# Performance work log

Hardware: AMD Instinct MI355X
Metric: run time of the kernel (lower is better)

The kernel has to match this reference:

```python
import jax, jax.numpy as jnp
import numpy as np

B, G, D, H, L, MLP = 64, 512, 384, 6, 12, 4
DH = D // H
MASK_RATIO = 0.6
KEEP_RATIO = 0.1
PAD_VAL = -1.0
START_VAL = 1.0
POS_HID = 128
NEG = -1e9


def setup_inputs() -> dict:
    key = jax.random.key(0)
    ks = jax.random.split(key, 24)
    s = 0.02
    inp = {
        "x": jax.random.normal(ks[0], (B, G, D), jnp.float32),
        "center_points": jax.random.normal(ks[1], (B, G, 3), jnp.float32),
        "mask_noise": jax.random.uniform(ks[2], (B, G), jnp.float32),
        # pos embedder MLP: 3 -> 128 -> D
        "pos_w1": jax.random.normal(ks[3], (3, POS_HID), jnp.float32) * s,
        "pos_b1": jnp.zeros((POS_HID,), jnp.float32),
        "pos_w2": jax.random.normal(ks[4], (POS_HID, D), jnp.float32) * s,
        "pos_b2": jnp.zeros((D,), jnp.float32),
        # stacked per-layer transformer params
        "ln1_w": jnp.ones((L, D), jnp.float32),
        "ln1_b": jnp.zeros((L, D), jnp.float32),
        "qkv_w": jax.random.normal(ks[5], (L, D, 3 * D), jnp.float32) * s,
        "qkv_b": jnp.zeros((L, 3 * D), jnp.float32),
        "proj_w": jax.random.normal(ks[6], (L, D, D), jnp.float32) * s,
        "proj_b": jnp.zeros((L, D), jnp.float32),
        "ln2_w": jnp.ones((L, D), jnp.float32),
        "ln2_b": jnp.zeros((L, D), jnp.float32),
        "fc1_w": jax.random.normal(ks[7], (L, D, MLP * D), jnp.float32) * s,
        "fc1_b": jnp.zeros((L, MLP * D), jnp.float32),
        "fc2_w": jax.random.normal(ks[8], (L, MLP * D, D), jnp.float32) * s,
        "fc2_b": jnp.zeros((L, D), jnp.float32),
        # final LayerNorm
        "norm_w": jnp.ones((D,), jnp.float32),
        "norm_b": jnp.zeros((D,), jnp.float32),
    }
    return inp


def _layer_norm(h, w, b, eps=1e-5):
    mu = jnp.mean(h, axis=-1, keepdims=True)
    var = jnp.mean(jnp.square(h - mu), axis=-1, keepdims=True)
    return (h - mu) * jax.lax.rsqrt(var + eps) * w + b


def _random_mask(center, noise):
    # padding tokens: all coords equal PAD_VAL
    pad = jnp.all(center == PAD_VAL, axis=-1)                      # [B, G] bool
    if MASK_RATIO == 0:
        return jnp.zeros(pad.shape, bool), pad
    n = (G - jnp.sum(pad.astype(jnp.int32), axis=-1))              # non-padding count
    k = (n.astype(jnp.float32) * KEEP_RATIO).astype(jnp.int32)     # kept-first tokens
    m = ((n - k).astype(jnp.float32) * MASK_RATIO).astype(jnp.int32)
    M = jnp.max(m)
    j = jnp.arange(G)[None, :]
    # shuffle region [k, n): pick m random slots (uniform subset via rank of noise)
    region = (j >= k[:, None]) & (j < n[:, None])
    u = jnp.where(region, noise, jnp.inf)
    rank = jnp.argsort(jnp.argsort(u, axis=-1), axis=-1)
    shuf = (rank < m[:, None]) & region
    # tail of ones: positions [n, n + M - m)
    tail = (j >= n[:, None]) & (j < (n + M - m)[:, None])
    return shuf | tail, pad


def _attention(h, qw, qb, pw, pb, bias):
    qkv = (h @ qw + qb).reshape(B, G, 3, H, DH).transpose(2, 0, 3, 1, 4)
    q, k, v = qkv[0], qkv[1], qkv[2]                               # [B, H, G, DH]
    s = jnp.einsum('bhqd,bhkd->bhqk', q, k) * (DH ** -0.5) + bias
    a = jax.nn.softmax(s, axis=-1)
    o = jnp.einsum('bhqk,bhkd->bhqd', a, v).transpose(0, 2, 1, 3).reshape(B, G, D)
    return o @ pw + pb


def _forward(x, center_points, mask_noise,
             pos_w1, pos_b1, pos_w2, pos_b2,
             ln1_w, ln1_b, qkv_w, qkv_b, proj_w, proj_b,
             ln2_w, ln2_b, fc1_w, fc1_b, fc2_w, fc2_b,
             norm_w, norm_b):
    # shift right + start token
    start = jnp.full((B, 1, D), START_VAL, x.dtype)
    x = jnp.concatenate([start, x[:, :-1, :]], axis=1)
    # positional embedding of shifted centers + start-token pos
    pos = jax.nn.gelu(center_points[:, :-1, :] @ pos_w1 + pos_b1, approximate=False) @ pos_w2 + pos_b2
    pos = jnp.concatenate([jnp.full((B, 1, D), START_VAL, x.dtype), pos], axis=1)
    # causal | (random column mask & ~eye) attention mask
    triu = jnp.triu(jnp.ones((G, G), bool), 1)
    rand_mask, pad = _random_mask(center_points, mask_noise)
    eye = jnp.eye(G, dtype=bool)
    attn_mask = triu[None, :, :] | (rand_mask[:, None, :] & ~eye[None, :, :])   # [B, G, G]
    bias = jnp.where(attn_mask | pad[:, None, :], NEG, 0.0)[:, None, :, :]      # [B,1,G,G]

    def block(h, p):
        l1w, l1b, qw, qb, pw, pb, l2w, l2b, f1w, f1b, f2w, f2b = p
        h = h + pos
        h = h + _attention(_layer_norm(h, l1w, l1b), qw, qb, pw, pb, bias)
        h = h + (jax.nn.gelu(_layer_norm(h, l2w, l2b) @ f1w + f1b, approximate=False) @ f2w + f2b)
        return h, None

    x, _ = jax.lax.scan(block, x, (ln1_w, ln1_b, qkv_w, qkv_b, proj_w, proj_b,
                                   ln2_w, ln2_b, fc1_w, fc1_b, fc2_w, fc2_b))
    x = _layer_norm(x, norm_w, norm_b)
    return x, pad, attn_mask


def reference(x, center_points, mask_noise,
              pos_w1, pos_b1, pos_w2, pos_b2,
              ln1_w, ln1_b, qkv_w, qkv_b, proj_w, proj_b,
              ln2_w, ln2_b, fc1_w, fc1_b, fc2_w, fc2_b,
              norm_w, norm_b):
    out, pad, attn_mask = _forward(x, center_points, mask_noise,
                                   pos_w1, pos_b1, pos_w2, pos_b2,
                                   ln1_w, ln1_b, qkv_w, qkv_b, proj_w, proj_b,
                                   ln2_w, ln2_b, fc1_w, fc1_b, fc2_w, fc2_b,
                                   norm_w, norm_b)
    # torch repeat_interleave over heads -> [B*H, G, G]
    return out, pad, jnp.repeat(attn_mask, H, axis=0)
```

## Files before the change

### kernel.cpp

```cpp
#include <hip/hip_runtime.h>
#include <math.h>

typedef _Float16 f16;
typedef f16 f16x8 __attribute__((ext_vector_type(8)));
typedef f16 f16v2 __attribute__((ext_vector_type(2)));
typedef float f32x4 __attribute__((ext_vector_type(4)));

#define NB 64
#define NG 512
#define ND 384
#define NH 6
#define NL 12
#define NDH 64
#define BG (NB * NG)
#define BGD (BG * ND)

#define OFF_WQKV   0
#define OFF_WPROJ  2654208
#define OFF_WFC1   3538944
#define OFF_WFC2   7077888
#define OFF_FLAGS  10616832
#define OFF_NKM    10625024
#define OFF_MMAX   10625216
#define OFF_POS    10625280
#define OFF_HID    23208192
#define OFF_Y      25305344
#define OFF_YBIG   31596800
#define OFF_QB     56762624
#define OFF_KB     63054080
#define OFF_VT     69345536
#define OFF_OB     75636992
#define OFF_W2T    81928448
#define OFF_HB     81953024

typedef __attribute__((address_space(3))) void lds_t;
typedef const __attribute__((address_space(1))) void gmem_t;
__device__ __forceinline__ void gload16(const void* g, void* l)
{
    __builtin_amdgcn_global_load_lds((gmem_t*)g, (lds_t*)l, 16, 0, 0);
}

__global__ __launch_bounds__(256)
void transpose_kernel(const float* __restrict__ src, f16* __restrict__ dst,
                      int K, int N)
{
    __shared__ float tile[32][33];
    const int l = blockIdx.z;
    const float* S = src + (size_t)l * K * N;
    f16* D = dst + (size_t)l * K * N;
    const int n0 = blockIdx.x * 32, k0 = blockIdx.y * 32;
    const int tx = threadIdx.x, ty = threadIdx.y;
#pragma unroll
    for (int i = 0; i < 32; i += 8)
        tile[ty + i][tx] = S[(size_t)(k0 + ty + i) * N + n0 + tx];
    __syncthreads();
#pragma unroll
    for (int i = 0; i < 32; i += 8)
        D[(size_t)(n0 + ty + i) * K + k0 + tx] = (f16)tile[tx][ty + i];
}

__global__ __launch_bounds__(256)
void dpos_a(const float* cen, const float* w1, const float* b1, f16* hid)
{
    const int idx = blockIdx.x * 256 + threadIdx.x;
    if (idx >= BG * 128) return;
    const int t = idx >> 7, k = idx & 127;
    const int g = t & (NG - 1);
    if (g == 0) { hid[idx] = (f16)0.f; return; }
    const float* c = cen + (size_t)(t - 1) * 3;
    const float hv = c[0] * w1[k] + c[1] * w1[128 + k] + c[2] * w1[256 + k] + b1[k];
    hid[idx] = (f16)(0.5f * hv * (1.0f + erff(hv * 0.70710678118654752f)));
}

__global__ __launch_bounds__(384)
void pos_fix(f16* pos)
{
    const int b = blockIdx.x;
    pos[((size_t)b * NG) * ND + threadIdx.x] = (f16)1.0f;
}

__global__ __launch_bounds__(512)
void dmask_a(const float* cen, float* pad_out, int* nkm)
{
    const int b = blockIdx.x, j = threadIdx.x;
    const float* c = cen + ((size_t)b * NG + j) * 3;
    const bool pad = (c[0] == -1.f) && (c[1] == -1.f) && (c[2] == -1.f);
    pad_out[b * NG + j] = pad ? 1.f : 0.f;
    if (j == 0) {
        int cnt = 0;
        for (int i = 0; i < NG; i++) {
            const float* ci = cen + ((size_t)b * NG + i) * 3;
            cnt += (ci[0] == -1.f && ci[1] == -1.f && ci[2] == -1.f) ? 1 : 0;
        }
        const int n = NG - cnt;
        const int k = (int)((float)n * 0.1f);
        const int m = (int)((float)(n - k) * 0.6f);
        nkm[b * 3] = n; nkm[b * 3 + 1] = k; nkm[b * 3 + 2] = m;
    }
}

__global__ void dmask_m(const int* nkm, int* Mmax)
{
    if (threadIdx.x == 0 && blockIdx.x == 0) {
        int M = 0;
        for (int b = 0; b < NB; b++) M = max(M, nkm[b * 3 + 2]);
        *Mmax = M;
    }
}

__global__ __launch_bounds__(512)
void dmask_b(const float* cen, const float* noi, const int* nkm,
             const int* Mmax, unsigned char* flags)
{
    const int b = blockIdx.x, j = threadIdx.x;
    const int n = nkm[b * 3], k = nkm[b * 3 + 1], m = nkm[b * 3 + 2];
    const int M = *Mmax;
    const float nz = noi[b * NG + j];
    const bool inreg = (j >= k) && (j < n);
    bool shuf = false;
    if (inreg) {
        int cnt = 0;
        for (int i = 0; i < NG; i++) {
            if (i < k || i >= n) continue;
            const float ui = noi[b * NG + i];
            cnt += (ui < nz) || (ui == nz && i < j);
        }
        shuf = cnt < m;
    }
    const float* c = cen + ((size_t)b * NG + j) * 3;
    const bool pad = (c[0] == -1.f) && (c[1] == -1.f) && (c[2] == -1.f);
    const bool tail = (j >= n) && (j < n + M - m);
    flags[b * NG + j] = (unsigned char)(((shuf | tail) ? 1 : 0) | (pad ? 2 : 0));
}

__global__ __launch_bounds__(512)
void flags_rep_kernel(const unsigned char* flags, float* mo)
{
    const int bq = blockIdx.x;
    const int b = bq >> 9, q = bq & (NG - 1);
    const int j = threadIdx.x;
    mo[(((size_t)(b * NH) * NG + q) * NG) + j] = (float)flags[b * NG + j];
}

__global__ __launch_bounds__(512)
void mask_out_kernel(float* mo)
{
    const int bq = blockIdx.x;
    const int b = bq >> 9, q = bq & (NG - 1);
    const int j = threadIdx.x;
    const unsigned char f =
        (unsigned char)mo[(((size_t)(b * NH) * NG + q) * NG) + j];
    const float val = ((q < j) || ((f & 1) && (q != j))) ? 1.0f : 0.0f;
#pragma unroll
    for (int h = 0; h < NH; h++)
        mo[(((size_t)(b * NH + h) * NG + q) * NG) + j] = val;
}

__global__ __launch_bounds__(256)
void h0_kernel(const float* x, const f16* pos, f16* h)
{
    const size_t i = (size_t)blockIdx.x * 256 + threadIdx.x;
    const int g = (int)((i / ND) & (NG - 1));
    const float xv = x[(g == 0) ? i : (i - ND)];
    const float base = (g == 0) ? 1.0f : xv;
    h[i] = (f16)(base + (float)pos[i]);
}

template<int MODE>
__global__ __launch_bounds__(256)
void lnb_kernel(const f16* __restrict__ h,
                const float* __restrict__ w, const float* __restrict__ bb,
                f16* __restrict__ y16, float* __restrict__ y32)
{
    __shared__ float red[4][64];
    const int wid = threadIdx.x >> 6;
    const int lane = threadIdx.x & 63;
    const int t = blockIdx.x * 4 + wid;
    const size_t base = (size_t)t * ND + lane;
    float v[6];
    float s = 0.f;
#pragma unroll
    for (int i = 0; i < 6; i++) {
        const float xv = (float)h[base + i * 64];
        v[i] = xv; s += xv;
    }
    red[wid][lane] = s;
    __syncthreads();
    for (int st = 32; st > 0; st >>= 1) {
        if (lane < st) red[wid][lane] += red[wid][lane + st];
        __syncthreads();
    }
    const float mu = red[wid][0] * (1.f / ND);
    float vs = 0.f;
#pragma unroll
    for (int i = 0; i < 6; i++) { const float d = v[i] - mu; vs += d * d; }
    __syncthreads();
    red[wid][lane] = vs;
    __syncthreads();
    for (int st = 32; st > 0; st >>= 1) {
        if (lane < st) red[wid][lane] += red[wid][lane + st];
        __syncthreads();
    }
    const float rstd = rsqrtf(red[wid][0] * (1.f / ND) + 1e-5f);
#pragma unroll
    for (int i = 0; i < 6; i++) {
        const float o = (v[i] - mu) * rstd * w[lane + i * 64] + bb[lane + i * 64];
        if constexpr (MODE == 2) y32[base + i * 64] = o;
        else                     y16[base + i * 64] = (f16)o;
    }
}

template<int MODE>
__global__ __launch_bounds__(256)
void gemm_kernel(const f16* __restrict__ A, const f16* __restrict__ Bt,
                 const float* __restrict__ bias, int K, int NT,
                 f16* __restrict__ hres, f16* __restrict__ out16,
                 f16* __restrict__ Qo, f16* __restrict__ Ko, f16* __restrict__ Vo)
{
    __shared__ f16 sA[128 * 64];
    __shared__ f16 sB[128 * 64];
    const int tid = threadIdx.x;
    const int w = tid >> 6, lane = tid & 63;
    const int lr = lane & 15, lg = lane >> 4;
    const int wm = w >> 1, wn = w & 1;
    const int N = NT * 128;

    const int nwg = gridDim.x;
    const int chunk = nwg >> 3;
    const int flat = (blockIdx.x & 7) * chunk + (blockIdx.x >> 3);
    const int m0 = (flat / NT) * 128;
    const int n0 = (flat % NT) * 128;

    f32x4 acc[4][4];
#pragma unroll
    for (int mf = 0; mf < 4; mf++)
#pragma unroll
        for (int nf = 0; nf < 4; nf++)
            acc[mf][nf] = (f32x4){0.f, 0.f, 0.f, 0.f};

    const int srow0 = w * 8 + (lane >> 3);
    const int scolB = (lane & 7) * 16;

    for (int k0 = 0; k0 < K; k0 += 64) {
        __syncthreads();
#pragma unroll
        for (int i = 0; i < 4; i++) {
            const int row = i * 32 + srow0;
            const int colB = scolB ^ ((row & 7) << 4);
            const char* ga = (const char*)(A + (size_t)(m0 + row) * K + k0) + colB;
            const char* gb = (const char*)(Bt + (size_t)(n0 + row) * K + k0) + colB;
            gload16(ga, (char*)sA + row * 128 + scolB);
            gload16(gb, (char*)sB + row * 128 + scolB);
        }
        __syncthreads();
#pragma unroll
        for (int kk = 0; kk < 64; kk += 32) {
            f16x8 af[4], bf[4];
#pragma unroll
            for (int mf = 0; mf < 4; mf++) {
                const int r = wm * 64 + mf * 16 + lr;
                const int cb = ((kk + lg * 8) * 2) ^ ((r & 7) << 4);
                af[mf] = *(const f16x8*)((const char*)sA + r * 128 + cb);
            }
#pragma unroll
            for (int nf = 0; nf < 4; nf++) {
                const int r = wn * 64 + nf * 16 + lr;
                const int cb = ((kk + lg * 8) * 2) ^ ((r & 7) << 4);
                bf[nf] = *(const f16x8*)((const char*)sB + r * 128 + cb);
            }
#pragma unroll
            for (int mf = 0; mf < 4; mf++)
#pragma unroll
                for (int nf = 0; nf < 4; nf++)
                    acc[mf][nf] = __builtin_amdgcn_mfma_f32_16x16x32_f16(
                        af[mf], bf[nf], acc[mf][nf], 0, 0, 0);
        }
    }

#pragma unroll
    for (int mf = 0; mf < 4; mf++) {
#pragma unroll
        for (int nf = 0; nf < 4; nf++) {
            const int n_g = n0 + wn * 64 + nf * 16 + lr;
            const float bv = bias[n_g];
#pragma unroll
            for (int r = 0; r < 4; r++) {
                const int m_g = m0 + wm * 64 + mf * 16 + lg * 4 + r;
                const float v = acc[mf][nf][r] + bv;
                const size_t oidx = (size_t)m_g * N + n_g;
                if constexpr (MODE == 1) {
                    hres[oidx] = (f16)((float)hres[oidx] + v);
                } else if constexpr (MODE == 2) {
                    const float ge = 0.5f * v * (1.0f + erff(v * 0.70710678118654752f));
                    out16[oidx] = (f16)ge;
                } else if constexpr (MODE == 3) {
                    out16[oidx] = (f16)v;
                } else {
                    const int which = n_g / ND;
                    const int rem = n_g - which * ND;
                    const int hh = rem >> 6, dh = rem & 63;
                    const int bb2 = m_g >> 9, gg = m_g & (NG - 1);
                    if (which == 0)
                        Qo[((size_t)(bb2 * NH + hh) * NG + gg) * NDH + dh] = (f16)v;
                    else if (which == 1)
                        Ko[((size_t)(bb2 * NH + hh) * NG + gg) * NDH + dh] = (f16)v;
                    else
                        Vo[((size_t)(bb2 * NH + hh) * NDH + dh) * NG + gg] = (f16)v;
                }
            }
        }
    }
}

template<int ADDPOS>
__global__ __launch_bounds__(512)
void gemmln_kernel(const f16* __restrict__ A, const f16* __restrict__ Bt,
                   const float* __restrict__ bias, int K,
                   f16* __restrict__ hres, const f16* __restrict__ posadd,
                   const float* __restrict__ lw, const float* __restrict__ lb,
                   f16* __restrict__ Y)
{
    __shared__ f16 sA[128 * 64];
    __shared__ f16 sB[384 * 64];
    __shared__ float part[2][128][2];
    const int tid = threadIdx.x;
    const int w = tid >> 6, lane = tid & 63;
    const int lr = lane & 15, lg = lane >> 4;
    const int vm = w >> 1, vn = w & 1;

    const int nwg = gridDim.x;
    const int chunk = nwg >> 3;
    const int m0 = ((blockIdx.x & 7) * chunk + (blockIdx.x >> 3)) * 128;

    f32x4 acc[2][12];
#pragma unroll
    for (int mf = 0; mf < 2; mf++)
#pragma unroll
        for (int nf = 0; nf < 12; nf++)
            acc[mf][nf] = (f32x4){0.f, 0.f, 0.f, 0.f};

    const int srowA = tid >> 3;
    const int scolB = (tid & 7) * 16;

    for (int k0 = 0; k0 < K; k0 += 64) {
        __syncthreads();
#pragma unroll
        for (int i = 0; i < 2; i++) {
            const int row = i * 64 + srowA;
            const int colB = scolB ^ ((row & 7) << 4);
            gload16((const char*)(A + (size_t)(m0 + row) * K + k0) + colB,
                    (char*)sA + row * 128 + scolB);
        }
#pragma unroll
        for (int i = 0; i < 6; i++) {
            const int row = i * 64 + srowA;
            const int colB = scolB ^ ((row & 7) << 4);
            gload16((const char*)(Bt + (size_t)row * K + k0) + colB,
                    (char*)sB + row * 128 + scolB);
        }
        __syncthreads();
#pragma unroll
        for (int kk = 0; kk < 64; kk += 32) {
            f16x8 af[2];
#pragma unroll
            for (int mf = 0; mf < 2; mf++) {
                const int r = vm * 32 + mf * 16 + lr;
                const int cb = ((kk + lg * 8) * 2) ^ ((r & 7) << 4);
                af[mf] = *(const f16x8*)((const char*)sA + r * 128 + cb);
            }
#pragma unroll
            for (int half = 0; half < 2; half++) {
                f16x8 bf[6];
#pragma unroll
                for (int j = 0; j < 6; j++) {
                    const int nf = half * 6 + j;
                    const int r = vn * 192 + nf * 16 + lr;
                    const int cb = ((kk + lg * 8) * 2) ^ ((r & 7) << 4);
                    bf[j] = *(const f16x8*)((const char*)sB + r * 128 + cb);
                }
#pragma unroll
                for (int mf = 0; mf < 2; mf++)
#pragma unroll
                    for (int j = 0; j < 6; j++)
                        acc[mf][half * 6 + j] = __builtin_amdgcn_mfma_f32_16x16x32_f16(
                            af[mf], bf[j], acc[mf][half * 6 + j], 0, 0, 0);
            }
        }
    }

    f16v2 hn[2][12][2];
    float rs[2][4], rq[2][4];
#pragma unroll
    for (int mf = 0; mf < 2; mf++)
#pragma unroll
        for (int r = 0; r < 4; r++) { rs[mf][r] = 0.f; rq[mf][r] = 0.f; }

#pragma unroll
    for (int mf = 0; mf < 2; mf++) {
#pragma unroll
        for (int nf = 0; nf < 12; nf++) {
            const int col = vn * 192 + nf * 16 + lr;
            const float bv = bias[col];
#pragma unroll
            for (int r = 0; r < 4; r++) {
                const int row_g = m0 + vm * 32 + mf * 16 + lg * 4 + r;
                const size_t oidx = (size_t)row_g * ND + col;
                float hv = (float)hres[oidx] + acc[mf][nf][r] + bv;
                if constexpr (ADDPOS) hv += (float)posadd[oidx];
                const f16 hf = (f16)hv;
                hn[mf][nf][r >> 1][r & 1] = hf;
                const float hff = (float)hf;
                rs[mf][r] += hff;
                rq[mf][r] += hff * hff;
            }
        }
    }
#pragma unroll
    for (int mf = 0; mf < 2; mf++)
#pragma unroll
        for (int r = 0; r < 4; r++) {
#pragma unroll
            for (int off = 1; off < 16; off <<= 1) {
                rs[mf][r] += __shfl_xor(rs[mf][r], off);
                rq[mf][r] += __shfl_xor(rq[mf][r], off);
            }
        }
    if (lr == 0) {
#pragma unroll
        for (int mf = 0; mf < 2; mf++)
#pragma unroll
            for (int r = 0; r < 4; r++) {
                const int rl = vm * 32 + mf * 16 + lg * 4 + r;
                part[vn][rl][0] = rs[mf][r];
                part[vn][rl][1] = rq[mf][r];
            }
    }
    __syncthreads();

    float mus[2][4], rstds[2][4];
#pragma unroll
    for (int mf = 0; mf < 2; mf++)
#pragma unroll
        for (int r = 0; r < 4; r++) {
            const int rl = vm * 32 + mf * 16 + lg * 4 + r;
            const float s = part[0][rl][0] + part[1][rl][0];
            const float q = part[0][rl][1] + part[1][rl][1];
            const float mu = s * (1.f / ND);
            const float var = q * (1.f / ND) - mu * mu;
            mus[mf][r] = mu;
            rstds[mf][r] = rsqrtf(var + 1e-5f);
        }

#pragma unroll
    for (int mf = 0; mf < 2; mf++) {
#pragma unroll
        for (int nf = 0; nf < 12; nf++) {
            const int col = vn * 192 + nf * 16 + lr;
            const float wl = lw[col];
            const float bl = lb[col];
#pragma unroll
            for (int r = 0; r < 4; r++) {
                const int row_g = m0 + vm * 32 + mf * 16 + lg * 4 + r;
                const size_t oidx = (size_t)row_g * ND + col;
                const f16 hf = hn[mf][nf][r >> 1][r & 1];
                hres[oidx] = hf;
                const float o = ((float)hf - mus[mf][r]) * rstds[mf][r] * wl + bl;
                Y[oidx] = (f16)o;
            }
        }
    }
}

__global__ __launch_bounds__(256)
void attn_kernel(const f16* __restrict__ Q, const f16* __restrict__ Kt,
                 const f16* __restrict__ V, const unsigned char* __restrict__ flags,
                 f16* __restrict__ O)
{
    __shared__ f16 sQ[128][72];
    __shared__ f16 sK[64][72];
    __shared__ f16 sV[64][72];
    __shared__ f16 sP[4][16][72];
    const int tid = threadIdx.x;
    const int w = tid >> 6, lane = tid & 63;
    const int lr = lane & 15, lg = lane >> 4;
    const int q0 = blockIdx.x * 128;
    const int bh = blockIdx.y;
    const int b = bh / NH, hh = bh - b * NH;
    const f16* Qg = Q + ((size_t)bh * NG + q0) * NDH;
    const f16* Kg = Kt + (size_t)bh * NG * NDH;
    const f16* Vg = V + (size_t)bh * NDH * NG;
    const unsigned char* fl = flags + b * NG;

#pragma unroll
    for (int i = 0; i < 4; i++) {
        const int c = tid + i * 256;
        const int r = c >> 3, cc = (c & 7) * 8;
        *(f16x8*)&sQ[r][cc] = *(const f16x8*)(Qg + r * NDH + cc);
    }
    __syncthreads();
    f16x8 aq[2][2];
#pragma unroll
    for (int hf = 0; hf < 2; hf++) {
        aq[hf][0] = *(const f16x8*)&sQ[hf * 64 + w * 16 + lr][lg * 8];
        aq[hf][1] = *(const f16x8*)&sQ[hf * 64 + w * 16 + lr][32 + lg * 8];
    }

    float m_run[2][4], l_run[2][4];
    f32x4 o[2][4];
#pragma unroll
    for (int hf = 0; hf < 2; hf++)
#pragma unroll
        for (int r = 0; r < 4; r++) {
            m_run[hf][r] = -INFINITY; l_run[hf][r] = 0.f;
            o[hf][r] = (f32x4){0.f, 0.f, 0.f, 0.f};
        }

    const int ntile = 2 * blockIdx.x + 2;
    for (int jt = 0; jt < ntile; jt++) {
        const int j0 = jt * 64;
        __syncthreads();
#pragma unroll
        for (int i = 0; i < 2; i++) {
            const int c = tid + i * 256;
            const int r = c >> 3, cc = (c & 7) * 8;
            *(f16x8*)&sK[r][cc] = *(const f16x8*)(Kg + (size_t)(j0 + r) * NDH + cc);
            *(f16x8*)&sV[r][cc] = *(const f16x8*)(Vg + (size_t)r * NG + j0 + cc);
        }
        __syncthreads();

#pragma unroll
        for (int hf = 0; hf < 2; hf++) {
            if (jt >= ntile - 1 + hf) continue;
            f32x4 s[4];
#pragma unroll
            for (int nf = 0; nf < 4; nf++) s[nf] = (f32x4){0.f, 0.f, 0.f, 0.f};
#pragma unroll
            for (int kf = 0; kf < 2; kf++) {
#pragma unroll
                for (int nf = 0; nf < 4; nf++) {
                    f16x8 bk = *(const f16x8*)&sK[nf * 16 + lr][kf * 32 + lg * 8];
                    s[nf] = __builtin_amdgcn_mfma_f32_16x16x32_f16(aq[hf][kf], bk, s[nf], 0, 0, 0);
                }
            }
#pragma unroll
            for (int nf = 0; nf < 4; nf++) {
                const int j_g = j0 + nf * 16 + lr;
                const unsigned char f = fl[j_g];
#pragma unroll
                for (int r = 0; r < 4; r++) {
                    const int q_g = q0 + hf * 64 + w * 16 + lg * 4 + r;
                    const bool masked = (q_g < j_g) || (f & 2) || ((f & 1) && (j_g != q_g));
                    s[nf][r] = s[nf][r] * 0.125f + (masked ? -1e9f : 0.f);
                }
            }
#pragma unroll
            for (int r = 0; r < 4; r++) {
                float mx = fmaxf(fmaxf(s[0][r], s[1][r]), fmaxf(s[2][r], s[3][r]));
#pragma unroll
                for (int off = 1; off < 16; off <<= 1) mx = fmaxf(mx, __shfl_xor(mx, off));
                const float nm = fmaxf(m_run[hf][r], mx);
                const float sc = __expf(m_run[hf][r] - nm);
                m_run[hf][r] = nm;
                l_run[hf][r] *= sc;
#pragma unroll
                for (int nf = 0; nf < 4; nf++) o[hf][nf][r] *= sc;
                float ls = 0.f;
#pragma unroll
                for (int nf = 0; nf < 4; nf++) {
                    const float p = __expf(s[nf][r] - nm);
                    ls += p;
                    sP[w][lg * 4 + r][nf * 16 + lr] = (f16)p;
                }
                l_run[hf][r] += ls;
            }
#pragma unroll
            for (int kf = 0; kf < 2; kf++) {
                f16x8 ap = *(const f16x8*)&sP[w][lr][kf * 32 + lg * 8];
#pragma unroll
                for (int nf = 0; nf < 4; nf++) {
                    f16x8 bv = *(const f16x8*)&sV[nf * 16 + lr][kf * 32 + lg * 8];
                    o[hf][nf] = __builtin_amdgcn_mfma_f32_16x16x32_f16(ap, bv, o[hf][nf], 0, 0, 0);
                }
            }
        }
    }

#pragma unroll
    for (int hf = 0; hf < 2; hf++) {
        float inv[4];
#pragma unroll
        for (int r = 0; r < 4; r++) {
            float l = l_run[hf][r];
#pragma unroll
            for (int off = 1; off < 16; off <<= 1) l += __shfl_xor(l, off);
            inv[r] = 1.f / l;
        }
#pragma unroll
        for (int nf = 0; nf < 4; nf++) {
#pragma unroll
            for (int r = 0; r < 4; r++) {
                const int q_g = q0 + hf * 64 + w * 16 + lg * 4 + r;
                const int dh = nf * 16 + lr;
                O[((size_t)(b * NG + q_g)) * ND + hh * NDH + dh] = (f16)(o[hf][nf][r] * inv[r]);
            }
        }
    }
}

extern "C" void kernel_launch(void* const* d_in, const int* in_sizes, int n_in,
                              void* d_out, int out_size, void* d_ws, size_t ws_size,
                              hipStream_t stream)
{
    (void)d_ws; (void)ws_size;

    static const int exp_sizes[21] = {
        12582912, 98304, 32768,
        384, 128, 49152, 384,
        4608, 4608,
        5308416, 13824,
        1769472, 4608,
        4608, 4608,
        7077888, 18432,
        7077888, 4608,
        384, 384
    };
    if (n_in != 21 || out_size != 113278976) return;
    for (int i = 0; i < 21; i++) if (in_sizes[i] != exp_sizes[i]) return;

    const float* x    = (const float*)d_in[0];
    const float* cen  = (const float*)d_in[1];
    const float* noi  = (const float*)d_in[2];
    const float* pw1  = (const float*)d_in[3];
    const float* pb1  = (const float*)d_in[4];
    const float* pw2  = (const float*)d_in[5];
    const float* pb2  = (const float*)d_in[6];
    const float* ln1w = (const float*)d_in[7];
    const float* ln1b = (const float*)d_in[8];
    const float* qkvw = (const float*)d_in[9];
    const float* qkvb = (const float*)d_in[10];
    const float* projw= (const float*)d_in[11];
    const float* projb= (const float*)d_in[12];
    const float* ln2w = (const float*)d_in[13];
    const float* ln2b = (const float*)d_in[14];
    const float* fc1w = (const float*)d_in[15];
    const float* fc1b = (const float*)d_in[16];
    const float* fc2w = (const float*)d_in[17];
    const float* fc2b = (const float*)d_in[18];
    const float* nw   = (const float*)d_in[19];
    const float* nb   = (const float*)d_in[20];

    float* out0    = (float*)d_out;
    float* pad_out = out0 + BGD;
    float* R       = pad_out + BG;

    f16* WqkvT  = (f16*)(R + OFF_WQKV);
    f16* WprojT = (f16*)(R + OFF_WPROJ);
    f16* Wfc1T  = (f16*)(R + OFF_WFC1);
    f16* Wfc2T  = (f16*)(R + OFF_WFC2);
    unsigned char* flags = (unsigned char*)(R + OFF_FLAGS);
    int* nkm  = (int*)(R + OFF_NKM);
    int* Mmax = (int*)(R + OFF_MMAX);
    f16* POS   = (f16*)(R + OFF_POS);
    f16* HID   = (f16*)(R + OFF_HID);
    f16* Y     = (f16*)(R + OFF_Y);
    f16* Ybig  = (f16*)(R + OFF_YBIG);
    f16* Qb    = (f16*)(R + OFF_QB);
    f16* Kb    = (f16*)(R + OFF_KB);
    f16* Vt    = (f16*)(R + OFF_VT);
    f16* Ob    = (f16*)(R + OFF_OB);
    f16* W2T   = (f16*)(R + OFF_W2T);
    f16* Hb    = (f16*)(R + OFF_HB);

    dim3 tb(32, 8);
    transpose_kernel<<<dim3(36, 12, NL), tb, 0, stream>>>(qkvw, WqkvT, 384, 1152);
    transpose_kernel<<<dim3(12, 12, NL), tb, 0, stream>>>(projw, WprojT, 384, 384);
    transpose_kernel<<<dim3(48, 12, NL), tb, 0, stream>>>(fc1w, Wfc1T, 384, 1536);
    transpose_kernel<<<dim3(12, 48, NL), tb, 0, stream>>>(fc2w, Wfc2T, 1536, 384);
    transpose_kernel<<<dim3(12, 4, 1),  tb, 0, stream>>>(pw2, W2T, 128, 384);

    dmask_a<<<NB, 512, 0, stream>>>(cen, pad_out, nkm);
    dmask_m<<<1, 64, 0, stream>>>(nkm, Mmax);
    dmask_b<<<NB, 512, 0, stream>>>(cen, noi, nkm, Mmax, flags);
    dpos_a<<<BG * 128 / 256, 256, 0, stream>>>(cen, pw1, pb1, HID);
    gemm_kernel<3><<<768, 256, 0, stream>>>(HID, W2T, pb2, 128, 3,
                                            nullptr, POS,
                                            nullptr, nullptr, nullptr);
    pos_fix<<<NB, 384, 0, stream>>>(POS);
    h0_kernel<<<BGD / 256, 256, 0, stream>>>(x, POS, Hb);

    lnb_kernel<1><<<BG / 4, 256, 0, stream>>>(Hb, ln1w, ln1b, Y, nullptr);

    for (int l = 0; l < NL; l++) {
        gemm_kernel<0><<<2304, 256, 0, stream>>>(Y, WqkvT + (size_t)l * 442368,
                                                 qkvb + l * 1152, 384, 9,
                                                 nullptr, nullptr,
                                                 Qb, Kb, Vt);
        attn_kernel<<<dim3(4, NB * NH), 256, 0, stream>>>(Qb, Kb, Vt, flags, Ob);
        gemmln_kernel<0><<<256, 512, 0, stream>>>(Ob, WprojT + (size_t)l * 147456,
                                                  projb + l * ND, 384,
                                                  Hb, nullptr,
                                                  ln2w + l * ND, ln2b + l * ND, Y);
        gemm_kernel<2><<<3072, 256, 0, stream>>>(Y, Wfc1T + (size_t)l * 589824,
                                                 fc1b + l * 1536, 384, 12,
                                                 nullptr, Ybig,
                                                 nullptr, nullptr, nullptr);
        if (l < NL - 1) {
            gemmln_kernel<1><<<256, 512, 0, stream>>>(Ybig, Wfc2T + (size_t)l * 589824,
                                                      fc2b + l * ND, 1536,
                                                      Hb, POS,
                                                      ln1w + (l + 1) * ND, ln1b + (l + 1) * ND, Y);
        } else {
            gemm_kernel<1><<<768, 256, 0, stream>>>(Ybig, Wfc2T + (size_t)l * 589824,
                                                    fc2b + l * ND, 1536, 3,
                                                    Hb, nullptr,
                                                    nullptr, nullptr, nullptr);
        }
    }

    lnb_kernel<2><<<BG / 4, 256, 0, stream>>>(Hb, nw, nb, nullptr, out0);
    flags_rep_kernel<<<BG, 512, 0, stream>>>(flags, R);
    mask_out_kernel<<<BG, 512, 0, stream>>>(R);
}
```

Baseline: 4.913 ms.

## Halve gemmln row tile to 64 and fuse final LayerNorm into last fc2

The fused GEMM+residual+LayerNorm kernel now processes 64 rows per block instead of 128, doubling the grid to 512 blocks so more CUs are covered and fewer accumulator registers are needed. The last layer's fc2 now also uses this fused kernel with an fp32 output mode that applies the final LayerNorm directly, removing a separate GEMM and LayerNorm pass. In exchange, each weight tile in shared memory is reused over fewer rows, so B-matrix loads double.

Measured after the change: 4.856 ms. No clear change (-1.2%).

```diff
diff --git a/kernel.cpp b/kernel.cpp
--- a/kernel.cpp
+++ b/kernel.cpp
@@ -312,17 +312,17 @@
     }
 }
 
-template<int ADDPOS>
+template<int ADDPOS, int OUT32>
 __global__ __launch_bounds__(512)
 void gemmln_kernel(const f16* __restrict__ A, const f16* __restrict__ Bt,
                    const float* __restrict__ bias, int K,
                    f16* __restrict__ hres, const f16* __restrict__ posadd,
                    const float* __restrict__ lw, const float* __restrict__ lb,
-                   f16* __restrict__ Y)
-{
-    __shared__ f16 sA[128 * 64];
+                   f16* __restrict__ Y, float* __restrict__ y32)
+{
+    __shared__ f16 sA[64 * 64];
     __shared__ f16 sB[384 * 64];
-    __shared__ float part[2][128][2];
+    __shared__ float part[2][64][2];
     const int tid = threadIdx.x;
     const int w = tid >> 6, lane = tid & 63;
     const int lr = lane & 15, lg = lane >> 4;
@@ -330,23 +330,20 @@
 
     const int nwg = gridDim.x;
     const int chunk = nwg >> 3;
-    const int m0 = ((blockIdx.x & 7) * chunk + (blockIdx.x >> 3)) * 128;
-
-    f32x4 acc[2][12];
-#pragma unroll
-    for (int mf = 0; mf < 2; mf++)
-#pragma unroll
-        for (int nf = 0; nf < 12; nf++)
-            acc[mf][nf] = (f32x4){0.f, 0.f, 0.f, 0.f};
+    const int m0 = ((blockIdx.x & 7) * chunk + (blockIdx.x >> 3)) * 64;
+
+    f32x4 acc[12];
+#pragma unroll
+    for (int nf = 0; nf < 12; nf++)
+        acc[nf] = (f32x4){0.f, 0.f, 0.f, 0.f};
 
     const int srowA = tid >> 3;
     const int scolB = (tid & 7) * 16;
 
     for (int k0 = 0; k0 < K; k0 += 64) {
         __syncthreads();
-#pragma unroll
-        for (int i = 0; i < 2; i++) {
-            const int row = i * 64 + srowA;
+        {
+            const int row = srowA;
             const int colB = scolB ^ ((row & 7) << 4);
             gload16((const char*)(A + (size_t)(m0 + row) * K + k0) + colB,
                     (char*)sA + row * 128 + scolB);
@@ -361,12 +358,11 @@
         __syncthreads();
 #pragma unroll
         for (int kk = 0; kk < 64; kk += 32) {
-            f16x8 af[2];
-#pragma unroll
-            for (int mf = 0; mf < 2; mf++) {
-                const int r = vm * 32 + mf * 16 + lr;
+            f16x8 af;
+            {
+                const int r = vm * 16 + lr;
                 const int cb = ((kk + lg * 8) * 2) ^ ((r & 7) << 4);
-                af[mf] = *(const f16x8*)((const char*)sA + r * 128 + cb);
+                af = *(const f16x8*)((const char*)sA + r * 128 + cb);
             }
 #pragma unroll
             for (int half = 0; half < 2; half++) {
@@ -379,92 +375,80 @@
                     bf[j] = *(const f16x8*)((const char*)sB + r * 128 + cb);
                 }
 #pragma unroll
-                for (int mf = 0; mf < 2; mf++)
-#pragma unroll
-                    for (int j = 0; j < 6; j++)
-                        acc[mf][half * 6 + j] = __builtin_amdgcn_mfma_f32_16x16x32_f16(
-                            af[mf], bf[j], acc[mf][half * 6 + j], 0, 0, 0);
-            }
-        }
-    }
-
-    f16v2 hn[2][12][2];
-    float rs[2][4], rq[2][4];
-#pragma unroll
-    for (int mf = 0; mf < 2; mf++)
-#pragma unroll
-        for (int r = 0; r < 4; r++) { rs[mf][r] = 0.f; rq[mf][r] = 0.f; }
-
-#pragma unroll
-    for (int mf = 0; mf < 2; mf++) {
-#pragma unroll
-        for (int nf = 0; nf < 12; nf++) {
-            const int col = vn * 192 + nf * 16 + lr;
-            const float bv = bias[col];
-#pragma unroll
-            for (int r = 0; r < 4; r++) {
-                const int row_g = m0 + vm * 32 + mf * 16 + lg * 4 + r;
-                const size_t oidx = (size_t)row_g * ND + col;
-                float hv = (float)hres[oidx] + acc[mf][nf][r] + bv;
-                if constexpr (ADDPOS) hv += (float)posadd[oidx];
-                const f16 hf = (f16)hv;
-                hn[mf][nf][r >> 1][r & 1] = hf;
-                const float hff = (float)hf;
-                rs[mf][r] += hff;
-                rq[mf][r] += hff * hff;
-            }
-        }
-    }
-#pragma unroll
-    for (int mf = 0; mf < 2; mf++)
+                for (int j = 0; j < 6; j++)
+                    acc[half * 6 + j] = __builtin_amdgcn_mfma_f32_16x16x32_f16(
+                        af, bf[j], acc[half * 6 + j], 0, 0, 0);
+            }
+        }
+    }
+
+    f16v2 hn[12][2];
+    float rs[4], rq[4];
+#pragma unroll
+    for (int r = 0; r < 4; r++) { rs[r] = 0.f; rq[r] = 0.f; }
+
+#pragma unroll
+    for (int nf = 0; nf < 12; nf++) {
+        const int col = vn * 192 + nf * 16 + lr;
+        const float bv = bias[col];
 #pragma unroll
         for (int r = 0; r < 4; r++) {
-#pragma unroll
-            for (int off = 1; off < 16; off <<= 1) {
-                rs[mf][r] += __shfl_xor(rs[mf][r], off);
-                rq[mf][r] += __shfl_xor(rq[mf][r], off);
-            }
-        }
+            const int row_g = m0 + vm * 16 + lg * 4 + r;
+            const size_t oidx = (size_t)row_g * ND + col;
+            float hv = (float)hres[oidx] + acc[nf][r] + bv;
+            if constexpr (ADDPOS) hv += (float)posadd[oidx];
+            const f16 hf = (f16)hv;
+            hn[nf][r >> 1][r & 1] = hf;
+            const float hff = (float)hf;
+            rs[r] += hff;
+            rq[r] += hff * hff;
+        }
+    }
+#pragma unroll
+    for (int r = 0; r < 4; r++) {
+#pragma unroll
+        for (int off = 1; off < 16; off <<= 1) {
+            rs[r] += __shfl_xor(rs[r], off);
+            rq[r] += __shfl_xor(rq[r], off);
+        }
+    }
     if (lr == 0) {
 #pragma unroll
-        for (int mf = 0; mf < 2; mf++)
-#pragma unroll
-            for (int r = 0; r < 4; r++) {
-                const int rl = vm * 32 + mf * 16 + lg * 4 + r;
-                part[vn][rl][0] = rs[mf][r];
-                part[vn][rl][1] = rq[mf][r];
-            }
+        for (int r = 0; r < 4; r++) {
+            const int rl = vm * 16 + lg * 4 + r;
+            part[vn][rl][0] = rs[r];
+            part[vn][rl][1] = rq[r];
+        }
     }
     __syncthreads();
 
-    float mus[2][4], rstds[2][4];
-#pragma unroll
-    for (int mf = 0; mf < 2; mf++)
+    float mus[4], rstds[4];
+#pragma unroll
+    for (int r = 0; r < 4; r++) {
+        const int rl = vm * 16 + lg * 4 + r;
+        const float s = part[0][rl][0] + part[1][rl][0];
+        const float q = part[0][rl][1] + part[1][rl][1];
+        const float mu = s * (1.f / ND);
+        const float var = q * (1.f / ND) - mu * mu;
+        mus[r] = mu;
+        rstds[r] = rsqrtf(var + 1e-5f);
+    }
+
+#pragma unroll
+    for (int nf = 0; nf < 12; nf++) {
+        const int col = vn * 192 + nf * 16 + lr;
+        const float wl = lw[col];
+        const float bl = lb[col];
 #pragma unroll
         for (int r = 0; r < 4; r++) {
-            const int rl = vm * 32 + mf * 16 + lg * 4 + r;
-            const float s = part[0][rl][0] + part[1][rl][0];
-            const float q = part[0][rl][1] + part[1][rl][1];
-            const float mu = s * (1.f / ND);
-            const float var = q * (1.f / ND) - mu * mu;
-            mus[mf][r] = mu;
-            rstds[mf][r] = rsqrtf(var + 1e-5f);
-        }
-
-#pragma unroll
-    for (int mf = 0; mf < 2; mf++) {
-#pragma unroll
-        for (int nf = 0; nf < 12; nf++) {
-            const int col = vn * 192 + nf * 16 + lr;
-            const float wl = lw[col];
-            const float bl = lb[col];
-#pragma unroll
-            for (int r = 0; r < 4; r++) {
-                const int row_g = m0 + vm * 32 + mf * 16 + lg * 4 + r;
-                const size_t oidx = (size_t)row_g * ND + col;
-                const f16 hf = hn[mf][nf][r >> 1][r & 1];
+            const int row_g = m0 + vm * 16 + lg * 4 + r;
+            const size_t oidx = (size_t)row_g * ND + col;
+            const f16 hf = hn[nf][r >> 1][r & 1];
+            const float o = ((float)hf - mus[r]) * rstds[r] * wl + bl;
+            if constexpr (OUT32) {
+                y32[oidx] = o;
+            } else {
                 hres[oidx] = hf;
-                const float o = ((float)hf - mus[mf][r]) * rstds[mf][r] * wl + bl;
                 Y[oidx] = (f16)o;
             }
         }
@@ -696,28 +680,30 @@
                                                  nullptr, nullptr,
                                                  Qb, Kb, Vt);
         attn_kernel<<<dim3(4, NB * NH), 256, 0, stream>>>(Qb, Kb, Vt, flags, Ob);
-        gemmln_kernel<0><<<256, 512, 0, stream>>>(Ob, WprojT + (size_t)l * 147456,
-                                                  projb + l * ND, 384,
-                                                  Hb, nullptr,
-                                                  ln2w + l * ND, ln2b + l * ND, Y);
+        gemmln_kernel<0, 0><<<512, 512, 0, stream>>>(Ob, WprojT + (size_t)l * 147456,
+                                                     projb + l * ND, 384,
+                                                     Hb, nullptr,
+                                                     ln2w + l * ND, ln2b + l * ND,
+                                                     Y, nullptr);
         gemm_kernel<2><<<3072, 256, 0, stream>>>(Y, Wfc1T + (size_t)l * 589824,
                                                  fc1b + l * 1536, 384, 12,
                                                  nullptr, Ybig,
                                                  nullptr, nullptr, nullptr);
         if (l < NL - 1) {
-            gemmln_kernel<1><<<256, 512, 0, stream>>>(Ybig, Wfc2T + (size_t)l * 589824,
-                                                      fc2b + l * ND, 1536,
-                                                      Hb, POS,
-                                                      ln1w + (l + 1) * ND, ln1b + (l + 1) * ND, Y);
+            gemmln_kernel<1, 0><<<512, 512, 0, stream>>>(Ybig, Wfc2T + (size_t)l * 589824,
+                                                         fc2b + l * ND, 1536,
+                                                         Hb, POS,
+                                                         ln1w + (l + 1) * ND, ln1b + (l + 1) * ND,
+                                                         Y, nullptr);
         } else {
-            gemm_kernel<1><<<768, 256, 0, stream>>>(Ybig, Wfc2T + (size_t)l * 589824,
-                                                    fc2b + l * ND, 1536, 3,
-                                                    Hb, nullptr,
-                                                    nullptr, nullptr, nullptr);
-        }
-    }
-
-    lnb_kernel<2><<<BG / 4, 256, 0, stream>>>(Hb, nw, nb, nullptr, out0);
+            gemmln_kernel<0, 1><<<512, 512, 0, stream>>>(Ybig, Wfc2T + (size_t)l * 589824,
+                                                         fc2b + l * ND, 1536,
+                                                         Hb, nullptr,
+                                                         nw, nb,
+                                                         nullptr, out0);
+        }
+    }
+
     flags_rep_kernel<<<BG, 512, 0, stream>>>(flags, R);
     mask_out_kernel<<<BG, 512, 0, stream>>>(R);
 }
```
